# Kernel tuning notes

Measured on AMD Instinct MI355X. Metric: run time of the kernel, lower is better.

## Reference

```python
import jax, jax.numpy as jnp
import numpy as np

EPS = 1e-6
NUM_HEADS = 2
DIM = 64
DIM_OUT = 128
SR = 4
SAMPLE_NUM = 784


def layer_norm(x, g, b, eps=1e-5):
    m = jnp.mean(x, -1, keepdims=True)
    v = jnp.mean((x - m) ** 2, -1, keepdims=True)
    return (x - m) * jax.lax.rsqrt(v + eps) * g + b


def gaussian_filt(x, kernel_size, sigma):
    # depthwise gaussian blur, x: [B, Ch, H, W]
    ch = x.shape[1]
    coord = jnp.arange(kernel_size, dtype=x.dtype)
    xg, yg = jnp.meshgrid(coord, coord, indexing='xy')
    mean = (kernel_size - 1) / 2.0
    var = sigma ** 2.0
    gk = jnp.exp(-((xg - mean) ** 2 + (yg - mean) ** 2) / (2.0 * var)) / (2.0 * np.pi * var)
    gk = gk / jnp.sum(gk)
    kernel = jnp.broadcast_to(gk[None, None], (ch, 1, kernel_size, kernel_size))
    pad = (kernel_size - 1) // 2
    return jax.lax.conv_general_dilated(
        x, kernel, (1, 1), [(pad, pad), (pad, pad)],
        dimension_numbers=('NCHW', 'OIHW', 'NCHW'), feature_group_count=ch)


def reconstruct_feature(feature, mask, kernel_size, sigma):
    if kernel_size <= 1:
        return feature
    feature = feature * mask
    out = gaussian_filt(jnp.concatenate([feature, mask], axis=1), kernel_size, sigma)
    fi = out[:, :-1]
    mi = out[:, -1:]
    fi = fi / (mi + EPS)
    fi = fi * (mi > 0).astype(feature.dtype)
    return feature + (1 - mask) * fi


def token2map(x, loc, H, W, kernel_size, sigma):
    # scatter tokens onto an HxW grid by rounded location, then gaussian-fill holes
    B, N, C = x.shape
    loc = jnp.clip(loc, 0, 1) * jnp.array([W - 1, H - 1], dtype=loc.dtype)
    loc = jnp.round(loc).astype(jnp.int32)
    idx = loc[..., 0] + loc[..., 1] * W + jnp.arange(B, dtype=jnp.int32)[:, None] * (H * W)
    src = jnp.concatenate([x, jnp.ones((B, N, 1), x.dtype)], axis=-1).reshape(B * N, C + 1)
    out = jax.ops.segment_sum(src, idx.reshape(-1), num_segments=B * H * W)
    out = out.reshape(B, H, W, C + 1).transpose(0, 3, 1, 2)
    feat, mask = out[:, :-1], out[:, -1:]
    feat = feat / (mask + EPS)
    mask = (mask > 0).astype(feat.dtype)
    feat = feat * mask
    return reconstruct_feature(feat, mask, kernel_size, sigma)


def grid_sample_bilinear(img, gx, gy):
    # F.grid_sample: bilinear, zeros padding, align_corners=False
    # img: [B, C, H, W]; gx, gy in [-1, 1]: [B, N]
    B, C, H, W = img.shape
    ix = ((gx + 1) * W - 1) / 2
    iy = ((gy + 1) * H - 1) / 2
    x0 = jnp.floor(ix)
    y0 = jnp.floor(iy)
    wx1 = ix - x0
    wy1 = iy - y0
    imgf = img.reshape(B, C, H * W)

    def corner(xc, yc, w):
        valid = (xc >= 0) & (xc < W) & (yc >= 0) & (yc < H)
        xi = jnp.clip(xc, 0, W - 1).astype(jnp.int32)
        yi = jnp.clip(yc, 0, H - 1).astype(jnp.int32)
        lin = (yi * W + xi)[:, None, :]                      # [B,1,N]
        v = jnp.take_along_axis(imgf, lin, axis=2)           # [B,C,N]
        return v * (w * valid)[:, None, :]

    out = (corner(x0, y0, (1 - wx1) * (1 - wy1))
           + corner(x0 + 1, y0, wx1 * (1 - wy1))
           + corner(x0, y0 + 1, (1 - wx1) * wy1)
           + corner(x0 + 1, y0 + 1, wx1 * wy1))
    return out.transpose(0, 2, 1)                            # [B,N,C]


def _forward(x, pos, pos_embed, noise_u, norm_g, norm_b, conf_w, conf_b,
             norm1_g, norm1_b, q_w, k_w, v_w, proj_w, proj_b, sr_w, sr_b,
             srnorm_g, srnorm_b, fc_w, fc_b, norm2_g, norm2_b,
             fc1_w, fc1_b, fc2_w, fc2_b, H, W, N_grid):
    B, N, C = x.shape
    # --- DownLayer: confidence + gumbel top-k over adaptive tokens ---
    conf = layer_norm(x, norm_g, norm_b) @ conf_w + conf_b            # [B,N,1]
    noise = -jnp.log(-jnp.log(noise_u + EPS) + EPS)                   # gumbel noise
    scores = (conf[:, N_grid:] + noise)[..., 0]                       # [B,N-N_grid]
    _, idx = jax.lax.top_k(scores, SAMPLE_NUM)                        # [B,k]
    x_down = jnp.concatenate(
        [x[:, :N_grid], jnp.take_along_axis(x[:, N_grid:], idx[:, :, None], axis=1)], axis=1)
    pos_down = jnp.concatenate(
        [pos[:, :N_grid], jnp.take_along_axis(pos[:, N_grid:], idx[:, :, None], axis=1)], axis=1)

    # --- MyBlock: fc(x) + sr-attention, then MLP (eval mode: dropouts off) ---
    Nd = x_down.shape[1]
    xn = layer_norm(x_down, norm1_g, norm1_b)
    xsn = layer_norm(x, norm1_g, norm1_b)
    q = xn @ q_w                                                      # [B,Nd,DIM_OUT]
    fmap = token2map(xsn, pos, H, W, SR - 1, 2.0)                     # [B,C,H,W]
    xs = jax.lax.conv_general_dilated(
        fmap, sr_w, (SR, SR), 'VALID',
        dimension_numbers=('NCHW', 'OIHW', 'NCHW')) + sr_b[None, :, None, None]
    xs = xs.reshape(B, C, -1).transpose(0, 2, 1)                      # [B,Ns,C]
    xs = layer_norm(xs, srnorm_g, srnorm_b)
    k = xs @ k_w
    v = xs @ v_w
    hd = DIM_OUT // NUM_HEADS
    qh = q.reshape(B, Nd, NUM_HEADS, hd).transpose(0, 2, 1, 3)
    kh = k.reshape(B, -1, NUM_HEADS, hd).transpose(0, 2, 1, 3)
    vh = v.reshape(B, -1, NUM_HEADS, hd).transpose(0, 2, 1, 3)
    scale = (DIM // NUM_HEADS) ** -0.5                                # head_dim from input dim per source
    attn = jax.nn.softmax(jnp.einsum('bhqd,bhkd->bhqk', qh, kh) * scale, axis=-1)
    o = jnp.einsum('bhqk,bhkd->bhqd', attn, vh).transpose(0, 2, 1, 3).reshape(B, Nd, DIM_OUT)
    o = o @ proj_w + proj_b
    x2 = x_down @ fc_w + fc_b + o                                     # use_fc branch (dim_out != dim), alpha=1
    xn2 = layer_norm(x2, norm2_g, norm2_b)
    x2 = x2 + (jax.nn.gelu(xn2 @ fc1_w + fc1_b, approximate=False) @ fc2_w + fc2_b)

    # --- get_pos_embed: bilinear grid_sample of pos_embed at pos_down ---
    Cp = pos_embed.shape[-1]
    pe = jnp.broadcast_to(pos_embed.reshape(1, H, W, Cp).transpose(0, 3, 1, 2), (B, Cp, H, W))
    g = pos_down * 2 - 1
    pos_feat = grid_sample_bilinear(pe, g[..., 0], g[..., 1])         # [B,Nd,Cp]
    return x2 + pos_feat


def setup_inputs() -> dict:
    key = jax.random.key(0)
    ks = jax.random.split(key, 16)
    B, N = 64, 3136
    N_grid = 49

    def w(k, shape, fan):
        return jax.random.normal(k, shape, jnp.float32) / np.sqrt(fan)

    d = {}
    d['x'] = jax.random.normal(ks[0], (B, N, DIM), jnp.float32)
    d['pos'] = jax.random.uniform(ks[1], (B, N, 2), jnp.float32)
    d['pos_embed'] = jax.random.normal(ks[2], (1, N, DIM_OUT), jnp.float32) * 0.02
    d['noise_u'] = jax.random.uniform(ks[3], (B, N - N_grid, 1), jnp.float32)
    d['norm_g'] = jnp.ones(DIM); d['norm_b'] = jnp.zeros(DIM)
    d['conf_w'] = w(ks[4], (DIM, 1), DIM); d['conf_b'] = jnp.zeros(1)
    d['norm1_g'] = jnp.ones(DIM); d['norm1_b'] = jnp.zeros(DIM)
    d['q_w'] = w(ks[5], (DIM, DIM_OUT), DIM)
    d['k_w'] = w(ks[6], (DIM, DIM_OUT), DIM)
    d['v_w'] = w(ks[7], (DIM, DIM_OUT), DIM)
    d['proj_w'] = w(ks[8], (DIM_OUT, DIM_OUT), DIM_OUT); d['proj_b'] = jnp.zeros(DIM_OUT)
    d['sr_w'] = w(ks[9], (DIM, DIM, SR, SR), DIM * SR * SR); d['sr_b'] = jnp.zeros(DIM)
    d['srnorm_g'] = jnp.ones(DIM); d['srnorm_b'] = jnp.zeros(DIM)
    d['fc_w'] = w(ks[10], (DIM, DIM_OUT), DIM); d['fc_b'] = jnp.zeros(DIM_OUT)
    d['norm2_g'] = jnp.ones(DIM_OUT); d['norm2_b'] = jnp.zeros(DIM_OUT)
    d['fc1_w'] = w(ks[11], (DIM_OUT, 4 * DIM_OUT), DIM_OUT); d['fc1_b'] = jnp.zeros(4 * DIM_OUT)
    d['fc2_w'] = w(ks[12], (4 * DIM_OUT, DIM_OUT), 4 * DIM_OUT); d['fc2_b'] = jnp.zeros(DIM_OUT)
    d['H'] = 56; d['W'] = 56; d['N_grid'] = N_grid
    return d


def reference(x, pos, pos_embed, noise_u, norm_g, norm_b, conf_w, conf_b,
              norm1_g, norm1_b, q_w, k_w, v_w, proj_w, proj_b, sr_w, sr_b,
              srnorm_g, srnorm_b, fc_w, fc_b, norm2_g, norm2_b,
              fc1_w, fc1_b, fc2_w, fc2_b, H, W, N_grid):
    return _forward(x, pos, pos_embed, noise_u, norm_g, norm_b, conf_w, conf_b,
                    norm1_g, norm1_b, q_w, k_w, v_w, proj_w, proj_b, sr_w, sr_b,
                    srnorm_g, srnorm_b, fc_w, fc_b, norm2_g, norm2_b,
                    fc1_w, fc1_b, fc2_w, fc2_b, H, W, N_grid)
```

## Files before the change

### kernel.cpp

```cpp
#include <hip/hip_runtime.h>
#include <math.h>

#define DEVINL __device__ __forceinline__

constexpr int B_ = 64;
constexpr int N_ = 3136;
constexpr int C_ = 64;
constexpr int NG = 49;
constexpr int NSAMP = 784;
constexpr int ND = NG + NSAMP;
constexpr int NREST = N_ - NG;
constexpr int H_ = 56, W_ = 56;
constexpr int HW = H_ * W_;
constexpr int BHW = B_ * HW;
constexpr int NS = 14 * 14;
constexpr int KPAD = 224;
constexpr float LN_EPS = 1e-5f;
constexpr float EPS6 = 1e-6f;

typedef __attribute__((ext_vector_type(8))) short short8;
typedef __attribute__((ext_vector_type(4))) float f32x4;

DEVINL unsigned short f2bf(float f) {
  unsigned int u = __float_as_uint(f);
  unsigned int r = u + 0x7FFFu + ((u >> 16) & 1u);
  return (unsigned short)(r >> 16);
}

DEVINL float gelu_fast(float v) {
  float x = v * 0.70710678118654752f;
  float ax = fabsf(x);
  float t = 1.f / fmaf(0.3275911f, ax, 1.f);
  float poly = t * fmaf(t, fmaf(t, fmaf(t, fmaf(t, 1.061405429f, -1.453152027f),
                        1.421413741f), -0.284496736f), 0.254829592f);
  float e = 1.f - poly * __expf(-x * x);
  float erfv = copysignf(e, x);
  return 0.5f * v * (1.f + erfv);
}

__global__ __launch_bounds__(256) void k_conf(
    const float* __restrict__ x, const float* __restrict__ ng, const float* __restrict__ nb,
    const float* __restrict__ cw, const float* __restrict__ cb,
    const float* __restrict__ nu, double* __restrict__ scores) {
  int t = blockIdx.x * 256 + threadIdx.x;
  if (t >= B_ * N_) return;
  int b = t / N_, n = t - b * N_;
  if (n < NG) return;
  const float4* row = (const float4*)(x + (size_t)t * C_);
  float v[C_];
#pragma unroll
  for (int i = 0; i < 16; ++i) {
    float4 r = row[i];
    v[4*i] = r.x; v[4*i+1] = r.y; v[4*i+2] = r.z; v[4*i+3] = r.w;
  }
  double sd = 0.0;
#pragma unroll
  for (int i = 0; i < C_; ++i) sd += (double)v[i];
  double md = sd * (1.0/64.0);
  double vd = 0.0;
#pragma unroll
  for (int i = 0; i < C_; ++i) { double d = (double)v[i] - md; vd += d * d; }
  vd *= (1.0/64.0);
  double rsd = 1.0 / sqrt(vd + 1e-5);
  double conf = (double)cb[0];
#pragma unroll
  for (int i = 0; i < C_; ++i) {
    double xnv = ((double)v[i] - md) * rsd;
    conf += (xnv * (double)ng[i] + (double)nb[i]) * (double)cw[i];
  }
  double u = (double)nu[(size_t)b * NREST + (n - NG)];
  double noise = -log(-log(u + 1e-6) + 1e-6);
  scores[(size_t)b * NREST + (n - NG)] = conf + noise;
}

constexpr int NB = 2048;

__global__ __launch_bounds__(256) void k_topk2(const double* __restrict__ scores,
                                               int* __restrict__ idx) {
  __shared__ double sk[NREST];
  __shared__ int hist[NB];
  __shared__ int bstart[NB];
  __shared__ int fill[NB];
  __shared__ unsigned short order[NREST];
  __shared__ float redmin[256], redmax[256];
  __shared__ int scanbuf[256];
  int b = blockIdx.x, tid = threadIdx.x;
  const double* sc = scores + (size_t)b * NREST;
  float lmin = 3.4e38f, lmax = -3.4e38f;
  for (int i = tid; i < NREST; i += 256) {
    double d = sc[i];
    sk[i] = d;
    float f = (float)d;
    lmin = fminf(lmin, f); lmax = fmaxf(lmax, f);
  }
  for (int i = tid; i < NB; i += 256) hist[i] = 0;
  redmin[tid] = lmin; redmax[tid] = lmax;
  __syncthreads();
  for (int s = 128; s > 0; s >>= 1) {
    if (tid < s) {
      redmin[tid] = fminf(redmin[tid], redmin[tid + s]);
      redmax[tid] = fmaxf(redmax[tid], redmax[tid + s]);
    }
    __syncthreads();
  }
  float fmn = redmin[0];
  float scale = (float)NB / fmaxf(redmax[0] - fmn, 1e-30f);
  for (int i = tid; i < NREST; i += 256) {
    float f = (float)sk[i];
    int bn = (int)((f - fmn) * scale);
    bn = bn < 0 ? 0 : (bn > NB - 1 ? NB - 1 : bn);
    atomicAdd(&hist[bn], 1);
  }
  __syncthreads();
  int base = tid * 8;
  int s_t = 0;
#pragma unroll
  for (int i = 0; i < 8; ++i) s_t += hist[base + i];
  scanbuf[tid] = s_t;
  __syncthreads();
  int val = s_t;
  for (int off = 1; off < 256; off <<= 1) {
    int other = (tid + off < 256) ? scanbuf[tid + off] : 0;
    __syncthreads();
    val += other;
    scanbuf[tid] = val;
    __syncthreads();
  }
  int run = val - s_t;
#pragma unroll
  for (int i = 7; i >= 0; --i) {
    bstart[base + i] = run;
    run += hist[base + i];
  }
  __syncthreads();
  for (int i = tid; i < NB; i += 256) fill[i] = bstart[i];
  __syncthreads();
  for (int i = tid; i < NREST; i += 256) {
    float f = (float)sk[i];
    int bn = (int)((f - fmn) * scale);
    bn = bn < 0 ? 0 : (bn > NB - 1 ? NB - 1 : bn);
    int pos = atomicAdd(&fill[bn], 1);
    order[pos] = (unsigned short)i;
  }
  __syncthreads();
  for (int i = tid; i < NREST; i += 256) {
    double ke = sk[i];
    float f = (float)ke;
    int bn = (int)((f - fmn) * scale);
    bn = bn < 0 ? 0 : (bn > NB - 1 ? NB - 1 : bn);
    int st = bstart[bn], m = hist[bn];
    int r = st;
    for (int p = st; p < st + m; ++p) {
      int j = order[p];
      double kj = sk[j];
      r += (int)((kj > ke) | ((kj == ke) & (j < i)));
    }
    if (r < NSAMP) idx[(size_t)b * NSAMP + r] = i;
  }
}

__global__ __launch_bounds__(256) void k_gather_ln(
    const float* __restrict__ x, const float* __restrict__ pos, const int* __restrict__ idx,
    const float* __restrict__ n1g, const float* __restrict__ n1b,
    float* __restrict__ xd, float* __restrict__ xn, float* __restrict__ pd) {
  int t = blockIdx.x * 256 + threadIdx.x;
  if (t >= B_ * ND) return;
  int b = t / ND, r = t - b * ND;
  int srcn = (r < NG) ? r : (NG + idx[(size_t)b * NSAMP + (r - NG)]);
  const float4* row = (const float4*)(x + ((size_t)b * N_ + srcn) * C_);
  float4* xdr = (float4*)(xd + (size_t)t * C_);
  float v[C_];
  float s = 0.f, ss = 0.f;
#pragma unroll
  for (int i = 0; i < 16; ++i) {
    float4 rr = row[i];
    xdr[i] = rr;
    v[4*i] = rr.x; v[4*i+1] = rr.y; v[4*i+2] = rr.z; v[4*i+3] = rr.w;
    s += rr.x + rr.y + rr.z + rr.w;
    ss += rr.x*rr.x + rr.y*rr.y + rr.z*rr.z + rr.w*rr.w;
  }
  float m = s * (1.f/64.f);
  float var = ss * (1.f/64.f) - m*m;
  float rs = rsqrtf(var + LN_EPS);
#pragma unroll
  for (int i = 0; i < C_; ++i)
    xn[(size_t)t * C_ + i] = (v[i] - m) * rs * n1g[i] + n1b[i];
  pd[(size_t)2*t]   = pos[((size_t)b * N_ + srcn) * 2];
  pd[(size_t)2*t+1] = pos[((size_t)b * N_ + srcn) * 2 + 1];
}

__global__ __launch_bounds__(256) void k_link(
    const float* __restrict__ pos, int* __restrict__ head, int* __restrict__ next) {
  int tok = blockIdx.x * 256 + threadIdx.x;
  if (tok >= B_ * N_) return;
  int b = tok / N_;
  double px = fmin(fmax((double)pos[(size_t)2*tok],   0.0), 1.0) * (double)(W_ - 1);
  double py = fmin(fmax((double)pos[(size_t)2*tok+1], 0.0), 1.0) * (double)(H_ - 1);
  int xi = (int)rint(px), yi = (int)rint(py);
  int p = b * HW + yi * W_ + xi;
  next[tok] = atomicExch(&head[p], tok);
}

__global__ __launch_bounds__(256) void k_accum(
    const float* __restrict__ x, const float* __restrict__ n1g, const float* __restrict__ n1b,
    const int* __restrict__ head, const int* __restrict__ next, float* __restrict__ S) {
  int gt = blockIdx.x * 256 + threadIdx.x;
  int p = gt >> 6, lane = gt & 63;
  if (p >= B_ * HW) return;
  float g = n1g[lane], bb = n1b[lane];
  float acc = 0.f, cnt = 0.f;
  int tok = head[p];
  while (tok >= 0) {
    float v = x[(size_t)tok * C_ + lane];
    float s = v, ss = v * v;
#pragma unroll
    for (int m = 32; m > 0; m >>= 1) {
      s += __shfl_xor(s, m);
      ss += __shfl_xor(ss, m);
    }
    float mean = s * (1.f/64.f);
    float var = ss * (1.f/64.f) - mean * mean;
    float rs = rsqrtf(var + LN_EPS);
    acc += (v - mean) * rs * g + bb;
    cnt += 1.f;
    tok = next[tok];
  }
  float* base = S + (size_t)p * 65;
  base[lane] = acc;
  if (lane == 0) base[64] = cnt;
}

__global__ __launch_bounds__(256) void k_transpose(const float* __restrict__ S,
                                                   float* __restrict__ T,
                                                   float* __restrict__ M) {
  __shared__ float ls[64 * 65];
  int g0 = blockIdx.x * 64;
  int b = g0 / HW, p0 = g0 - b * HW;
  const float4* src = (const float4*)(S + (size_t)g0 * 65);
  for (int i = threadIdx.x; i < (64 * 65) / 4; i += 256)
    *(float4*)&ls[i * 4] = src[i];
  __syncthreads();
  for (int i = threadIdx.x; i < 64 * 64; i += 256) {
    int c = i >> 6, px = i & 63;
    T[((size_t)(b * 64 + c)) * HW + p0 + px] = ls[px * 65 + c];
  }
  for (int i = threadIdx.x; i < 64; i += 256)
    M[(size_t)g0 + i] = ls[i * 65 + 64];
}

__global__ __launch_bounds__(256) void k_coef(const float* __restrict__ M, float* __restrict__ Kc) {
  int t = blockIdx.x * 256 + threadIdx.x;
  if (t >= BHW) return;
  int b = t / HW, p = t - b * HW;
  int y = p / W_, x = p - y * W_;
  const float* Mb = M + (size_t)b * HW;
  const float e1 = 0.882496902584595f;
  const float e2 = 0.778800783071405f;
  const float Z = 1.f + 4.f * (e1 + e2);
  float m0 = Mb[p];
  float mb0 = m0 > 0.f ? 1.f : 0.f;
  float cfac = mb0 / (m0 + EPS6);
  float sc[9];
  float mi = 0.f;
  int q = 0;
#pragma unroll
  for (int dy = -1; dy <= 1; ++dy) {
#pragma unroll
    for (int dx = -1; dx <= 1; ++dx) {
      int ny = y + dy, nx = x + dx;
      bool in = (ny >= 0 && ny < H_ && nx >= 0 && nx < W_);
      float w = ((dx == 0 && dy == 0) ? 1.f : ((dx*dx + dy*dy) == 1 ? e1 : e2)) / Z;
      float mm = in ? Mb[ny * W_ + nx] : 0.f;
      float mb = mm > 0.f ? 1.f : 0.f;
      mi += w * mb;
      sc[q] = in ? (w * mb / (mm + EPS6)) : 0.f;
      ++q;
    }
  }
  float outer = (1.f - mb0) * ((mi > 0.f ? 1.f : 0.f) / (mi + EPS6));
#pragma unroll
  for (int qq = 0; qq < 9; ++qq) {
    float cq = outer * sc[qq];
    if (qq == 4) cq += cfac;
    Kc[(size_t)qq * BHW + t] = cq;
  }
}

__global__ __launch_bounds__(256) void k_filter2(
    const float* __restrict__ T, const float* __restrict__ Kc, float* __restrict__ P) {
  int plane = blockIdx.x;
  int b = plane >> 6, c = plane & 63;
  int tid = threadIdx.x;
  const float* Tp = T + (size_t)plane * HW;
  const float* Kb = Kc + (size_t)b * HW;
  for (int p0 = 0; p0 < HW; p0 += 256) {
    int p = p0 + tid;
    if (p < HW) {
      int y = p / W_, x = p - y * W_;
      float acc = 0.f;
      int q = 0;
#pragma unroll
      for (int dy = -1; dy <= 1; ++dy) {
#pragma unroll
        for (int dx = -1; dx <= 1; ++dx) {
          int ny = y + dy; ny = ny < 0 ? 0 : (ny > H_ - 1 ? H_ - 1 : ny);
          int nx = x + dx; nx = nx < 0 ? 0 : (nx > W_ - 1 ? W_ - 1 : nx);
          acc += Kb[(size_t)q * BHW + p] * Tp[ny * W_ + nx];
          ++q;
        }
      }
      int j = (y >> 2) * 14 + (x >> 2);
      int colb = ((y & 3) << 2) + (x & 3);
      P[((size_t)(b * NS + j)) * 1024 + c * 16 + colb] = acc;
    }
  }
}

__global__ __launch_bounds__(256) void k_wtp(const float* __restrict__ srw,
                                             unsigned short* __restrict__ Wcp) {
  int t = blockIdx.x * 256 + threadIdx.x;
  if (t >= 65536) return;
  int j = t & 7;
  int n = (t >> 3) & 63;
  int s = (t >> 9) & 15;
  int ch = t >> 13;
  int k = ch * 128 + (s >> 2) * 32 + (s & 3) * 8 + j;
  int ci = k >> 4, r = k & 15;
  Wcp[t] = f2bf(srw[(((size_t)n * 64 + ci) << 4) + r]);
}

__global__ __launch_bounds__(256) void k_wpack(const float* __restrict__ W1, const float* __restrict__ W2,
    unsigned short* __restrict__ W1q, unsigned short* __restrict__ W2q) {
  int t = blockIdx.x * 256 + threadIdx.x;
  if (t >= 65536) return;
  {
    int j = t & 7;
    int nl = (t >> 3) & 63;
    int s = (t >> 9) & 15;
    int hh = t >> 13;
    int k = (s >> 2) * 32 + (s & 3) * 8 + j;
    int n = hh * 64 + nl;
    W1q[t] = f2bf(W1[(size_t)k * 512 + n]);
  }
  {
    int j = t & 7;
    int n = (t >> 3) & 127;
    int s = (t >> 10) & 7;
    int hh = t >> 13;
    int k = hh * 64 + (s >> 2) * 32 + (s & 3) * 8 + j;
    W2q[t] = f2bf(W2[(size_t)k * 128 + n]);
  }
}

__global__ __launch_bounds__(256) void k_conv(
    const float* __restrict__ P, const unsigned short* __restrict__ Wcp,
    const float* __restrict__ bias, const float* __restrict__ sg,
    const float* __restrict__ sb, float* __restrict__ xsn) {
  __shared__ __align__(16) unsigned short sA[64 * 128];
  __shared__ __align__(16) unsigned short sW[8192];
  int bm = blockIdx.x * 64;
  int tid = threadIdx.x;
  int wv = tid >> 6, lane = tid & 63, quad = lane >> 4, l16 = lane & 15;

  const short8* gw = (const short8*)Wcp;
  short8* dw = (short8*)sW;

  short8 rw[4];
  float4 fa[4][2];
#pragma unroll
  for (int i = 0; i < 4; ++i) rw[i] = gw[i * 256 + tid];
#pragma unroll
  for (int i = 0; i < 4; ++i) {
    int u = i * 256 + tid;
    int row = u >> 4, ck = u & 15;
    const float* src = P + (size_t)(bm + row) * 1024 + ck * 8;
    fa[i][0] = *(const float4*)src;
    fa[i][1] = *(const float4*)(src + 4);
  }

  f32x4 acc[4];
#pragma unroll
  for (int ct = 0; ct < 4; ++ct) acc[ct] = (f32x4){0.f, 0.f, 0.f, 0.f};

  for (int ch = 0; ch < 8; ++ch) {
#pragma unroll
    for (int i = 0; i < 4; ++i) {
      dw[i * 256 + tid] = rw[i];
      int u = i * 256 + tid;
      int row = u >> 4, ck = u & 15;
      short8 p;
      p[0]=(short)f2bf(fa[i][0].x); p[1]=(short)f2bf(fa[i][0].y);
      p[2]=(short)f2bf(fa[i][0].z); p[3]=(short)f2bf(fa[i][0].w);
      p[4]=(short)f2bf(fa[i][1].x); p[5]=(short)f2bf(fa[i][1].y);
      p[6]=(short)f2bf(fa[i][1].z); p[7]=(short)f2bf(fa[i][1].w);
      *(short8*)&sA[row * 128 + (((ck ^ row) & 15) << 3)] = p;
    }
    __syncthreads();
    if (ch < 7) {
      int wbase = (ch + 1) * 1024;
#pragma unroll
      for (int i = 0; i < 4; ++i) rw[i] = gw[wbase + i * 256 + tid];
#pragma unroll
      for (int i = 0; i < 4; ++i) {
        int u = i * 256 + tid;
        int row = u >> 4, ck = u & 15;
        const float* src = P + (size_t)(bm + row) * 1024 + (ch + 1) * 128 + ck * 8;
        fa[i][0] = *(const float4*)src;
        fa[i][1] = *(const float4*)(src + 4);
      }
    }
#pragma unroll
    for (int kc = 0; kc < 4; ++kc) {
      int row = wv * 16 + l16;
      int ck = kc * 4 + quad;
      short8 af = *(const short8*)&sA[row * 128 + (((ck ^ row) & 15) << 3)];
      int s = kc * 4 + quad;
#pragma unroll
      for (int ct = 0; ct < 4; ++ct) {
        short8 bf = *(const short8*)&sW[(s * 64 + ct * 16 + l16) << 3];
        acc[ct] = __builtin_amdgcn_mfma_f32_16x16x32_bf16(af, bf, acc[ct], 0, 0, 0);
      }
    }
    __syncthreads();
  }
  float vv[4][4];
  float rsum[4], rss[4];
#pragma unroll
  for (int r = 0; r < 4; ++r) { rsum[r] = 0.f; rss[r] = 0.f; }
#pragma unroll
  for (int ct = 0; ct < 4; ++ct)
#pragma unroll
    for (int r = 0; r < 4; ++r) {
      float v = acc[ct][r] + bias[ct * 16 + l16];
      vv[ct][r] = v;
      rsum[r] += v;
      rss[r] += v * v;
    }
#pragma unroll
  for (int m = 1; m < 16; m <<= 1)
#pragma unroll
    for (int r = 0; r < 4; ++r) {
      rsum[r] += __shfl_xor(rsum[r], m);
      rss[r]  += __shfl_xor(rss[r], m);
    }
  float mean[4], rsl[4];
#pragma unroll
  for (int r = 0; r < 4; ++r) {
    mean[r] = rsum[r] * (1.f/64.f);
    float var = rss[r] * (1.f/64.f) - mean[r] * mean[r];
    rsl[r] = rsqrtf(var + LN_EPS);
  }
#pragma unroll
  for (int ct = 0; ct < 4; ++ct)
#pragma unroll
    for (int r = 0; r < 4; ++r) {
      int row = bm + wv * 16 + quad * 4 + r;
      int col = ct * 16 + l16;
      xsn[(size_t)row * 64 + col] = (vv[ct][r] - mean[r]) * rsl[r] * sg[col] + sb[col];
    }
}

__global__ __launch_bounds__(256) void k_gemm(
    const float* __restrict__ A, const float* __restrict__ Bw,
    const float* __restrict__ bias, const float* __restrict__ add,
    float* __restrict__ Cout, int M, int N, int K) {
  __shared__ float sA[16][68];
  __shared__ float sB[16][64];
  int bm = blockIdx.x * 64, bn = blockIdx.y * 64;
  int tid = threadIdx.x;
  int tx = tid & 15, ty = tid >> 4;
  float acc[4][4] = {{0.f}};
  for (int k0 = 0; k0 < K; k0 += 16) {
    int e = tid << 2;
    int am = e >> 4, ak = e & 15;
    float4 a4 = *(const float4*)(A + (size_t)(bm + am) * K + k0 + ak);
    sA[ak + 0][am] = a4.x; sA[ak + 1][am] = a4.y; sA[ak + 2][am] = a4.z; sA[ak + 3][am] = a4.w;
    int bk = e >> 6, nn = e & 63;
    float4 b4 = *(const float4*)(Bw + (size_t)(k0 + bk) * N + bn + nn);
    *(float4*)&sB[bk][nn] = b4;
    __syncthreads();
#pragma unroll
    for (int kk = 0; kk < 16; ++kk) {
      float a[4], bb[4];
#pragma unroll
      for (int i = 0; i < 4; ++i) a[i] = sA[kk][ty * 4 + i];
#pragma unroll
      for (int i = 0; i < 4; ++i) bb[i] = sB[kk][tx * 4 + i];
#pragma unroll
      for (int i = 0; i < 4; ++i)
#pragma unroll
        for (int jj = 0; jj < 4; ++jj) acc[i][jj] += a[i] * bb[jj];
    }
    __syncthreads();
  }
#pragma unroll
  for (int i = 0; i < 4; ++i) {
    int row = bm + ty * 4 + i;
#pragma unroll
    for (int jj = 0; jj < 4; ++jj) {
      int col = bn + tx * 4 + jj;
      float v = acc[i][jj];
      if (bias) v += bias[col];
      if (add) v += add[(size_t)row * N + col];
      Cout[(size_t)row * N + col] = v;
    }
  }
}

__global__ __launch_bounds__(256) void k_mlp(
    const float* __restrict__ A, const float* __restrict__ gg, const float* __restrict__ gb,
    const unsigned short* __restrict__ W1q, const float* __restrict__ b1,
    const unsigned short* __restrict__ W2q, const float* __restrict__ b2,
    float* __restrict__ out) {
  __shared__ __align__(16) unsigned short sW1[8192];
  __shared__ __align__(16) unsigned short sW2[8192];
  __shared__ __align__(16) unsigned short sH[4][16 * 64];
  int bm = blockIdx.x * 64;
  int tid = threadIdx.x;
  int wv = tid >> 6, lane = tid & 63, quad = lane >> 4, l16 = lane & 15;

  const short8* g1 = (const short8*)W1q;
  const short8* g2 = (const short8*)W2q;
  short8* d1 = (short8*)sW1;
  short8* d2 = (short8*)sW2;

  short8 r1[4], r2[4];
#pragma unroll
  for (int i = 0; i < 4; ++i) {
    r1[i] = g1[i * 256 + tid];
    r2[i] = g2[i * 256 + tid];
  }

  int row = bm + wv * 16 + l16;
  const float* arow = A + (size_t)row * 128 + quad * 8;
  float av[4][8];
  float s = 0.f, ss = 0.f;
#pragma unroll
  for (int kc = 0; kc < 4; ++kc) {
    float4 a = *(const float4*)(arow + kc * 32);
    float4 c = *(const float4*)(arow + kc * 32 + 4);
    av[kc][0]=a.x; av[kc][1]=a.y; av[kc][2]=a.z; av[kc][3]=a.w;
    av[kc][4]=c.x; av[kc][5]=c.y; av[kc][6]=c.z; av[kc][7]=c.w;
    s += a.x+a.y+a.z+a.w + c.x+c.y+c.z+c.w;
    ss += a.x*a.x+a.y*a.y+a.z*a.z+a.w*a.w + c.x*c.x+c.y*c.y+c.z*c.z+c.w*c.w;
  }
  s += __shfl_xor(s, 16);  ss += __shfl_xor(ss, 16);
  s += __shfl_xor(s, 32);  ss += __shfl_xor(ss, 32);
  float m = s * (1.f/128.f);
  float var = ss * (1.f/128.f) - m * m;
  float rs = rsqrtf(var + LN_EPS);
  short8 af[4];
#pragma unroll
  for (int kc = 0; kc < 4; ++kc) {
    int c0 = kc * 32 + quad * 8;
    float4 ga = *(const float4*)(gg + c0);
    float4 gc = *(const float4*)(gg + c0 + 4);
    float4 ba = *(const float4*)(gb + c0);
    float4 bc = *(const float4*)(gb + c0 + 4);
    af[kc][0] = (short)f2bf((av[kc][0]-m)*rs*ga.x + ba.x);
    af[kc][1] = (short)f2bf((av[kc][1]-m)*rs*ga.y + ba.y);
    af[kc][2] = (short)f2bf((av[kc][2]-m)*rs*ga.z + ba.z);
    af[kc][3] = (short)f2bf((av[kc][3]-m)*rs*ga.w + ba.w);
    af[kc][4] = (short)f2bf((av[kc][4]-m)*rs*gc.x + bc.x);
    af[kc][5] = (short)f2bf((av[kc][5]-m)*rs*gc.y + bc.y);
    af[kc][6] = (short)f2bf((av[kc][6]-m)*rs*gc.z + bc.z);
    af[kc][7] = (short)f2bf((av[kc][7]-m)*rs*gc.w + bc.w);
  }

  f32x4 oacc[8];
#pragma unroll
  for (int ct = 0; ct < 8; ++ct) oacc[ct] = (f32x4){0.f, 0.f, 0.f, 0.f};

  for (int hh = 0; hh < 8; ++hh) {
#pragma unroll
    for (int i = 0; i < 4; ++i) {
      d1[i * 256 + tid] = r1[i];
      d2[i * 256 + tid] = r2[i];
    }
    __syncthreads();
    if (hh < 7) {
      int base = (hh + 1) * 1024;
#pragma unroll
      for (int i = 0; i < 4; ++i) {
        r1[i] = g1[base + i * 256 + tid];
        r2[i] = g2[base + i * 256 + tid];
      }
    }
    f32x4 acc1[4];
#pragma unroll
    for (int ct = 0; ct < 4; ++ct) acc1[ct] = (f32x4){0.f, 0.f, 0.f, 0.f};
#pragma unroll
    for (int kc = 0; kc < 4; ++kc) {
      int sidx = kc * 4 + quad;
#pragma unroll
      for (int ct = 0; ct < 4; ++ct) {
        short8 bf = *(const short8*)&sW1[(sidx * 64 + ct * 16 + l16) << 3];
        acc1[ct] = __builtin_amdgcn_mfma_f32_16x16x32_bf16(af[kc], bf, acc1[ct], 0, 0, 0);
      }
    }
#pragma unroll
    for (int ct = 0; ct < 4; ++ct)
#pragma unroll
      for (int r = 0; r < 4; ++r) {
        float v = acc1[ct][r] + b1[hh * 64 + ct * 16 + l16];
        v = gelu_fast(v);
        int rit = quad * 4 + r;
        int col = ct * 16 + l16;
        int ck = (col >> 3) ^ (rit & 7);
        sH[wv][rit * 64 + ((ck & 7) << 3) + (col & 7)] = f2bf(v);
      }
#pragma unroll
    for (int kg = 0; kg < 2; ++kg) {
      int ckh = kg * 4 + quad;
      short8 hf = *(const short8*)&sH[wv][l16 * 64 + (((ckh ^ (l16 & 7)) & 7) << 3)];
      int sidx = kg * 4 + quad;
#pragma unroll
      for (int ct = 0; ct < 8; ++ct) {
        short8 bf = *(const short8*)&sW2[(sidx * 128 + ct * 16 + l16) << 3];
        oacc[ct] = __builtin_amdgcn_mfma_f32_16x16x32_bf16(hf, bf, oacc[ct], 0, 0, 0);
      }
    }
    __syncthreads();
  }
#pragma unroll
  for (int ct = 0; ct < 8; ++ct)
#pragma unroll
    for (int r = 0; r < 4; ++r) {
      int orow = bm + wv * 16 + quad * 4 + r;
      int col = ct * 16 + l16;
      out[(size_t)orow * 128 + col] += oacc[ct][r] + b2[col];
    }
}

__global__ __launch_bounds__(256) void k_attn(const float* __restrict__ q,
    const float* __restrict__ kg, const float* __restrict__ vg, float* __restrict__ o) {
  __shared__ __align__(16) unsigned short ldsKP[14848];
  __shared__ __align__(16) unsigned short ldsV[16128];
  int blk = blockIdx.x;
  int chunk = blk % 14;
  int bh = blk / 14;
  int h = bh & 1, b = bh >> 1;
  int tid = threadIdx.x;
  int wv = tid >> 6, lane = tid & 63;
  int quad = lane >> 4, l16 = lane & 15;

  const float* kb = kg + (size_t)b * NS * 128 + h * 64;
  const float* vb = vg + (size_t)b * NS * 128 + h * 64;

  for (int t = tid; t < KPAD * 8; t += 256) {
    int key = t >> 3, ck = t & 7;
    short8 pk, pv;
    if (key < NS) {
      const float* ksrc = kb + (size_t)key * 128 + ck * 8;
      const float* vsrc = vb + (size_t)key * 128 + ck * 8;
      float4 a = *(const float4*)ksrc;
      float4 c = *(const float4*)(ksrc + 4);
      pk[0]=(short)f2bf(a.x); pk[1]=(short)f2bf(a.y); pk[2]=(short)f2bf(a.z); pk[3]=(short)f2bf(a.w);
      pk[4]=(short)f2bf(c.x); pk[5]=(short)f2bf(c.y); pk[6]=(short)f2bf(c.z); pk[7]=(short)f2bf(c.w);
      float4 e = *(const float4*)vsrc;
      float4 g = *(const float4*)(vsrc + 4);
      pv[0]=(short)f2bf(e.x); pv[1]=(short)f2bf(e.y); pv[2]=(short)f2bf(e.z); pv[3]=(short)f2bf(e.w);
      pv[4]=(short)f2bf(g.x); pv[5]=(short)f2bf(g.y); pv[6]=(short)f2bf(g.z); pv[7]=(short)f2bf(g.w);
    } else {
      pk = (short8)0; pv = (short8)0;
    }
    *(short8*)&ldsKP[key * 64 + ((ck ^ (key & 7)) << 3)] = pk;
    *(short8*)&ldsV[key * 72 + ck * 8] = pv;
  }

  int qrow = chunk * 64 + wv * 16 + l16;
  int qrowc = qrow < ND ? qrow : ND - 1;
  const float* qsrc = q + ((size_t)b * ND + qrowc) * 128 + h * 64 + quad * 8;
  short8 aq0, aq1;
  {
    float4 a = *(const float4*)qsrc;
    float4 c = *(const float4*)(qsrc + 4);
    aq0[0]=(short)f2bf(a.x); aq0[1]=(short)f2bf(a.y); aq0[2]=(short)f2bf(a.z); aq0[3]=(short)f2bf(a.w);
    aq0[4]=(short)f2bf(c.x); aq0[5]=(short)f2bf(c.y); aq0[6]=(short)f2bf(c.z); aq0[7]=(short)f2bf(c.w);
    float4 e = *(const float4*)(qsrc + 32);
    float4 g = *(const float4*)(qsrc + 36);
    aq1[0]=(short)f2bf(e.x); aq1[1]=(short)f2bf(e.y); aq1[2]=(short)f2bf(e.z); aq1[3]=(short)f2bf(e.w);
    aq1[4]=(short)f2bf(g.x); aq1[5]=(short)f2bf(g.y); aq1[6]=(short)f2bf(g.z); aq1[7]=(short)f2bf(g.w);
  }
  __syncthreads();

  f32x4 acc[14];
#pragma unroll
  for (int ct = 0; ct < 14; ++ct) {
    int key = ct * 16 + l16;
    short8 bk0 = *(const short8*)&ldsKP[key * 64 + ((quad ^ (key & 7)) << 3)];
    short8 bk1 = *(const short8*)&ldsKP[key * 64 + (((4 + quad) ^ (key & 7)) << 3)];
    f32x4 z = {0.f, 0.f, 0.f, 0.f};
    z = __builtin_amdgcn_mfma_f32_16x16x32_bf16(aq0, bk0, z, 0, 0, 0);
    z = __builtin_amdgcn_mfma_f32_16x16x32_bf16(aq1, bk1, z, 0, 0, 0);
    acc[ct] = z;
  }

  const float scale = 0.17677669529663687f;
  float rmax[4] = {-1e30f, -1e30f, -1e30f, -1e30f};
#pragma unroll
  for (int ct = 0; ct < 14; ++ct) {
    bool msk = (ct * 16 + l16) >= NS;
#pragma unroll
    for (int r = 0; r < 4; ++r) {
      float sv = msk ? -1e30f : acc[ct][r] * scale;
      acc[ct][r] = sv;
      rmax[r] = fmaxf(rmax[r], sv);
    }
  }
#pragma unroll
  for (int m = 1; m < 16; m <<= 1)
#pragma unroll
    for (int r = 0; r < 4; ++r) rmax[r] = fmaxf(rmax[r], __shfl_xor(rmax[r], m));
  float rsum[4] = {0.f, 0.f, 0.f, 0.f};
#pragma unroll
  for (int ct = 0; ct < 14; ++ct)
#pragma unroll
    for (int r = 0; r < 4; ++r) {
      float e = __expf(acc[ct][r] - rmax[r]);
      acc[ct][r] = e;
      rsum[r] += e;
    }
#pragma unroll
  for (int m = 1; m < 16; m <<= 1)
#pragma unroll
    for (int r = 0; r < 4; ++r) rsum[r] += __shfl_xor(rsum[r], m);
  float rinv[4];
#pragma unroll
  for (int r = 0; r < 4; ++r) rinv[r] = 1.f / rsum[r];

  __syncthreads();

#pragma unroll
  for (int ct = 0; ct < 14; ++ct)
#pragma unroll
    for (int r = 0; r < 4; ++r) {
      int prow = wv * 16 + quad * 4 + r;
      ldsKP[prow * 232 + ct * 16 + l16] = f2bf(acc[ct][r] * rinv[r]);
    }
  __syncthreads();

  f32x4 oacc[4];
#pragma unroll
  for (int ot = 0; ot < 4; ++ot) oacc[ot] = (f32x4){0.f, 0.f, 0.f, 0.f};
#pragma unroll
  for (int kc = 0; kc < 7; ++kc) {
    short8 ap = *(const short8*)&ldsKP[(wv * 16 + l16) * 232 + kc * 32 + quad * 8];
    int keybase = kc * 32 + quad * 8;
#pragma unroll
    for (int ot = 0; ot < 4; ++ot) {
      int dcol = ot * 16 + l16;
      short8 bv;
#pragma unroll
      for (int j = 0; j < 8; ++j) bv[j] = (short)ldsV[(keybase + j) * 72 + dcol];
      oacc[ot] = __builtin_amdgcn_mfma_f32_16x16x32_bf16(ap, bv, oacc[ot], 0, 0, 0);
    }
  }

#pragma unroll
  for (int ot = 0; ot < 4; ++ot)
#pragma unroll
    for (int r = 0; r < 4; ++r) {
      int rowg = chunk * 64 + wv * 16 + quad * 4 + r;
      if (rowg < ND)
        o[((size_t)b * ND + rowg) * 128 + h * 64 + ot * 16 + l16] = oacc[ot][r];
    }
}

__global__ __launch_bounds__(256) void k_posfeat(const float* __restrict__ pd,
    const float* __restrict__ pe, float* __restrict__ out) {
  int t = blockIdx.x * 256 + threadIdx.x;
  int row = t >> 5, lane = t & 31;
  if (row >= B_ * ND) return;
  float gx = pd[(size_t)2*row] * 2.f - 1.f;
  float gy = pd[(size_t)2*row+1] * 2.f - 1.f;
  float ix = ((gx + 1.f) * 56.f - 1.f) * 0.5f;
  float iy = ((gy + 1.f) * 56.f - 1.f) * 0.5f;
  float x0 = floorf(ix), y0 = floorf(iy);
  float wx1 = ix - x0, wy1 = iy - y0;
  float wx0 = 1.f - wx1, wy0 = 1.f - wy1;
  float4 acc = make_float4(0.f, 0.f, 0.f, 0.f);
#pragma unroll
  for (int cy = 0; cy < 2; ++cy) {
#pragma unroll
    for (int cx = 0; cx < 2; ++cx) {
      float xc = x0 + (float)cx, yc = y0 + (float)cy;
      float wgt = (cx ? wx1 : wx0) * (cy ? wy1 : wy0);
      bool valid = (xc >= 0.f) && (xc < 56.f) && (yc >= 0.f) && (yc < 56.f);
      if (valid) {
        int lin = (int)yc * 56 + (int)xc;
        float4 pv = ((const float4*)(pe + (size_t)lin * 128))[lane];
        acc.x += wgt * pv.x; acc.y += wgt * pv.y;
        acc.z += wgt * pv.z; acc.w += wgt * pv.w;
      }
    }
  }
  float4* op = (float4*)(out + (size_t)row * 128) + lane;
  float4 cur = *op;
  cur.x += acc.x; cur.y += acc.y; cur.z += acc.z; cur.w += acc.w;
  *op = cur;
}

extern "C" void kernel_launch(void* const* d_in, const int* in_sizes, int n_in,
                              void* d_out, int out_size, void* d_ws, size_t ws_size,
                              hipStream_t stream) {
  const float* x      = (const float*)d_in[0];
  const float* pos    = (const float*)d_in[1];
  const float* pe     = (const float*)d_in[2];
  const float* nu     = (const float*)d_in[3];
  const float* norm_g = (const float*)d_in[4];
  const float* norm_b = (const float*)d_in[5];
  const float* conf_w = (const float*)d_in[6];
  const float* conf_b = (const float*)d_in[7];
  const float* n1g    = (const float*)d_in[8];
  const float* n1b    = (const float*)d_in[9];
  const float* q_w    = (const float*)d_in[10];
  const float* k_w    = (const float*)d_in[11];
  const float* v_w    = (const float*)d_in[12];
  const float* proj_w = (const float*)d_in[13];
  const float* proj_b = (const float*)d_in[14];
  const float* sr_w   = (const float*)d_in[15];
  const float* sr_b   = (const float*)d_in[16];
  const float* srn_g  = (const float*)d_in[17];
  const float* srn_b  = (const float*)d_in[18];
  const float* fc_w   = (const float*)d_in[19];
  const float* fc_b   = (const float*)d_in[20];
  const float* n2g    = (const float*)d_in[21];
  const float* n2b    = (const float*)d_in[22];
  const float* fc1_w  = (const float*)d_in[23];
  const float* fc1_b  = (const float*)d_in[24];
  const float* fc2_w  = (const float*)d_in[25];
  const float* fc2_b  = (const float*)d_in[26];

  char* ws = (char*)d_ws;
  double*         scores = (double*)(ws + 0);
  int*            idx    = (int*)(ws + 1605632);
  float*          xd     = (float*)(ws + 1835008);
  float*          xn     = (float*)(ws + 15728640);
  float*          pd     = (float*)(ws + 29491200);
  float*          qb     = (float*)(ws + 30408704);
  float*          ob     = (float*)(ws + 58720256);
  unsigned short* Wcp    = (unsigned short*)(ws + 86507520);
  unsigned short* W1p    = (unsigned short*)(ws + 86769664);
  unsigned short* W2p    = (unsigned short*)(ws + 86900736);
  char*           big    = ws + 87031808;
  float*          S      = (float*)big;
  float*          T      = qb;
  float*          Kc     = (float*)(big + 52183040);
  float*          P      = (float*)big;
  float*          xs_n   = (float*)(big + 62619648);
  float*          kbuf   = (float*)(big + 65830912);
  float*          vbuf   = (float*)(big + 72253440);
  float*          Mbuf   = (float*)(big + 78675968);
  int*            head   = (int*)(big + 79478784);
  int*            nxt    = (int*)(big + 80281600);
  float*          O2     = qb;
  float*          out    = (float*)d_out;

  k_conf<<<(B_ * N_) / 256, 256, 0, stream>>>(x, norm_g, norm_b, conf_w, conf_b, nu, scores);
  k_topk2<<<B_, 256, 0, stream>>>(scores, idx);
  k_gather_ln<<<(B_ * ND + 255) / 256, 256, 0, stream>>>(x, pos, idx, n1g, n1b, xd, xn, pd);
  hipMemsetAsync(head, 0xFF, (size_t)B_ * HW * sizeof(int), stream);
  k_link<<<(B_ * N_ + 255) / 256, 256, 0, stream>>>(pos, head, nxt);
  k_accum<<<(B_ * HW * 64) / 256, 256, 0, stream>>>(x, n1g, n1b, head, nxt, S);
  k_transpose<<<BHW / 64, 256, 0, stream>>>(S, T, Mbuf);
  k_coef<<<BHW / 256, 256, 0, stream>>>(Mbuf, Kc);
  k_filter2<<<B_ * 64, 256, 0, stream>>>(T, Kc, P);
  k_wtp<<<65536 / 256, 256, 0, stream>>>(sr_w, Wcp);
  k_wpack<<<65536 / 256, 256, 0, stream>>>(fc1_w, fc2_w, W1p, W2p);
  k_conv<<<B_ * NS / 64, 256, 0, stream>>>(P, Wcp, sr_b, srn_g, srn_b, xs_n);
  dim3 g_kv(B_ * NS / 64, 2);
  k_gemm<<<g_kv, 256, 0, stream>>>(xs_n, k_w, nullptr, nullptr, kbuf, B_ * NS, 128, 64);
  k_gemm<<<g_kv, 256, 0, stream>>>(xs_n, v_w, nullptr, nullptr, vbuf, B_ * NS, 128, 64);
  dim3 g_row(B_ * ND / 64, 2);
  k_gemm<<<g_row, 256, 0, stream>>>(xn, q_w, nullptr, nullptr, qb, B_ * ND, 128, 64);
  k_attn<<<B_ * 2 * 14, 256, 0, stream>>>(qb, kbuf, vbuf, ob);
  k_gemm<<<g_row, 256, 0, stream>>>(ob, proj_w, proj_b, nullptr, O2, B_ * ND, 128, 128);
  k_gemm<<<g_row, 256, 0, stream>>>(xd, fc_w, fc_b, O2, out, B_ * ND, 128, 64);
  k_mlp<<<B_ * ND / 64, 256, 0, stream>>>(out, n2g, n2b, W1p, fc1_b, W2p, fc2_b, out);
  k_posfeat<<<(B_ * ND * 32) / 256, 256, 0, stream>>>(pd, pe, out);
}
```

Baseline: 570.8 us.

## Fuse proj and fc GEMMs into one kernel; widen MLP blocks to 128 rows

The attention projection GEMM and the fc shortcut GEMM are merged into one kernel, k_x2, that computes both products per tile and writes their sum directly. This removes the intermediate O2 buffer round trip through memory and one launch. Separately, k_mlp now uses 512 threads covering 128 rows per block. Each block's weight staging into shared memory is shared across twice as many rows, and the ragged last block is handled with row clamping and store guards.

```diff
diff --git a/kernel.cpp b/kernel.cpp
--- a/kernel.cpp
+++ b/kernel.cpp
@@ -15,6 +15,7 @@
 constexpr int BHW = B_ * HW;
 constexpr int NS = 14 * 14;
 constexpr int KPAD = 224;
+constexpr int NROW = B_ * ND;
 constexpr float LN_EPS = 1e-5f;
 constexpr float EPS6 = 1e-6f;
 
@@ -507,15 +508,80 @@
   }
 }
 
-__global__ __launch_bounds__(256) void k_mlp(
+__global__ __launch_bounds__(256) void k_x2(
+    const float* __restrict__ ob, const float* __restrict__ pw, const float* __restrict__ pb,
+    const float* __restrict__ xd, const float* __restrict__ fw, const float* __restrict__ fb,
+    float* __restrict__ out) {
+  __shared__ float sA[16][68];
+  __shared__ float sB[16][64];
+  int bm = blockIdx.x * 64, bn = blockIdx.y * 64;
+  int tid = threadIdx.x;
+  int tx = tid & 15, ty = tid >> 4;
+  int e = tid << 2;
+  int am = e >> 4, ak = e & 15;
+  int bk = e >> 6, nn = e & 63;
+  float accP[4][4] = {{0.f}};
+  for (int k0 = 0; k0 < 128; k0 += 16) {
+    float4 a4 = *(const float4*)(ob + (size_t)(bm + am) * 128 + k0 + ak);
+    sA[ak + 0][am] = a4.x; sA[ak + 1][am] = a4.y; sA[ak + 2][am] = a4.z; sA[ak + 3][am] = a4.w;
+    float4 b4 = *(const float4*)(pw + (size_t)(k0 + bk) * 128 + bn + nn);
+    *(float4*)&sB[bk][nn] = b4;
+    __syncthreads();
+#pragma unroll
+    for (int kk = 0; kk < 16; ++kk) {
+      float a[4], bb[4];
+#pragma unroll
+      for (int i = 0; i < 4; ++i) a[i] = sA[kk][ty * 4 + i];
+#pragma unroll
+      for (int i = 0; i < 4; ++i) bb[i] = sB[kk][tx * 4 + i];
+#pragma unroll
+      for (int i = 0; i < 4; ++i)
+#pragma unroll
+        for (int jj = 0; jj < 4; ++jj) accP[i][jj] += a[i] * bb[jj];
+    }
+    __syncthreads();
+  }
+  float accF[4][4] = {{0.f}};
+  for (int k0 = 0; k0 < 64; k0 += 16) {
+    float4 a4 = *(const float4*)(xd + (size_t)(bm + am) * 64 + k0 + ak);
+    sA[ak + 0][am] = a4.x; sA[ak + 1][am] = a4.y; sA[ak + 2][am] = a4.z; sA[ak + 3][am] = a4.w;
+    float4 b4 = *(const float4*)(fw + (size_t)(k0 + bk) * 128 + bn + nn);
+    *(float4*)&sB[bk][nn] = b4;
+    __syncthreads();
+#pragma unroll
+    for (int kk = 0; kk < 16; ++kk) {
+      float a[4], bb[4];
+#pragma unroll
+      for (int i = 0; i < 4; ++i) a[i] = sA[kk][ty * 4 + i];
+#pragma unroll
+      for (int i = 0; i < 4; ++i) bb[i] = sB[kk][tx * 4 + i];
+#pragma unroll
+      for (int i = 0; i < 4; ++i)
+#pragma unroll
+        for (int jj = 0; jj < 4; ++jj) accF[i][jj] += a[i] * bb[jj];
+    }
+    __syncthreads();
+  }
+#pragma unroll
+  for (int i = 0; i < 4; ++i) {
+    int row = bm + ty * 4 + i;
+#pragma unroll
+    for (int jj = 0; jj < 4; ++jj) {
+      int col = bn + tx * 4 + jj;
+      out[(size_t)row * 128 + col] = accF[i][jj] + fb[col] + (accP[i][jj] + pb[col]);
+    }
+  }
+}
+
+__global__ __launch_bounds__(512) void k_mlp(
     const float* __restrict__ A, const float* __restrict__ gg, const float* __restrict__ gb,
     const unsigned short* __restrict__ W1q, const float* __restrict__ b1,
     const unsigned short* __restrict__ W2q, const float* __restrict__ b2,
     float* __restrict__ out) {
   __shared__ __align__(16) unsigned short sW1[8192];
   __shared__ __align__(16) unsigned short sW2[8192];
-  __shared__ __align__(16) unsigned short sH[4][16 * 64];
-  int bm = blockIdx.x * 64;
+  __shared__ __align__(16) unsigned short sH[8][16 * 64];
+  int bm = blockIdx.x * 128;
   int tid = threadIdx.x;
   int wv = tid >> 6, lane = tid & 63, quad = lane >> 4, l16 = lane & 15;
 
@@ -524,15 +590,16 @@
   short8* d1 = (short8*)sW1;
   short8* d2 = (short8*)sW2;
 
-  short8 r1[4], r2[4];
-#pragma unroll
-  for (int i = 0; i < 4; ++i) {
-    r1[i] = g1[i * 256 + tid];
-    r2[i] = g2[i * 256 + tid];
+  short8 r1[2], r2[2];
+#pragma unroll
+  for (int i = 0; i < 2; ++i) {
+    r1[i] = g1[i * 512 + tid];
+    r2[i] = g2[i * 512 + tid];
   }
 
   int row = bm + wv * 16 + l16;
-  const float* arow = A + (size_t)row * 128 + quad * 8;
+  int rowc = row < NROW ? row : NROW - 1;
+  const float* arow = A + (size_t)rowc * 128 + quad * 8;
   float av[4][8];
   float s = 0.f, ss = 0.f;
 #pragma unroll
@@ -573,17 +640,17 @@
 
   for (int hh = 0; hh < 8; ++hh) {
 #pragma unroll
-    for (int i = 0; i < 4; ++i) {
-      d1[i * 256 + tid] = r1[i];
-      d2[i * 256 + tid] = r2[i];
+    for (int i = 0; i < 2; ++i) {
+      d1[i * 512 + tid] = r1[i];
+      d2[i * 512 + tid] = r2[i];
     }
     __syncthreads();
     if (hh < 7) {
       int base = (hh + 1) * 1024;
 #pragma unroll
-      for (int i = 0; i < 4; ++i) {
-        r1[i] = g1[base + i * 256 + tid];
-        r2[i] = g2[base + i * 256 + tid];
+      for (int i = 0; i < 2; ++i) {
+        r1[i] = g1[base + i * 512 + tid];
+        r2[i] = g2[base + i * 512 + tid];
       }
     }
     f32x4 acc1[4];
@@ -628,7 +695,8 @@
     for (int r = 0; r < 4; ++r) {
       int orow = bm + wv * 16 + quad * 4 + r;
       int col = ct * 16 + l16;
-      out[(size_t)orow * 128 + col] += oacc[ct][r] + b2[col];
+      if (orow < NROW)
+        out[(size_t)orow * 128 + col] += oacc[ct][r] + b2[col];
     }
 }
 
@@ -854,7 +922,6 @@
   float*          Mbuf   = (float*)(big + 78675968);
   int*            head   = (int*)(big + 79478784);
   int*            nxt    = (int*)(big + 80281600);
-  float*          O2     = qb;
   float*          out    = (float*)d_out;
 
   k_conf<<<(B_ * N_) / 256, 256, 0, stream>>>(x, norm_g, norm_b, conf_w, conf_b, nu, scores);
@@ -875,8 +942,7 @@
   dim3 g_row(B_ * ND / 64, 2);
   k_gemm<<<g_row, 256, 0, stream>>>(xn, q_w, nullptr, nullptr, qb, B_ * ND, 128, 64);
   k_attn<<<B_ * 2 * 14, 256, 0, stream>>>(qb, kbuf, vbuf, ob);
-  k_gemm<<<g_row, 256, 0, stream>>>(ob, proj_w, proj_b, nullptr, O2, B_ * ND, 128, 128);
-  k_gemm<<<g_row, 256, 0, stream>>>(xd, fc_w, fc_b, O2, out, B_ * ND, 128, 64);
-  k_mlp<<<B_ * ND / 64, 256, 0, stream>>>(out, n2g, n2b, W1p, fc1_b, W2p, fc2_b, out);
+  k_x2<<<g_row, 256, 0, stream>>>(ob, proj_w, proj_b, xd, fc_w, fc_b, out);
+  k_mlp<<<(NROW + 127) / 128, 512, 0, stream>>>(out, n2g, n2b, W1p, fc1_b, W2p, fc2_b, out);
   k_posfeat<<<(B_ * ND * 32) / 256, 256, 0, stream>>>(pd, pe, out);
 }
```

After: 529.4 us. 7.3% less time.
